# Performance work log

Hardware: AMD Instinct MI355X
Metric: run time of the kernel (lower is better)

Reference implementation:

```python
import jax, jax.numpy as jnp
import numpy as np

# Static multi-level feature-map geometry (h, w) per level.
SPATIAL_SHAPES = np.array([[92, 92], [46, 46], [23, 23], [12, 12]], dtype=np.int32)
_AREAS = SPATIAL_SHAPES[:, 0] * SPATIAL_SHAPES[:, 1]
LEVEL_START = np.concatenate([[0], np.cumsum(_AREAS)[:-1]]).astype(np.int32)
LEN_IN = int(_AREAS.sum())  # 11253
N_HEADS, N_LEVELS, N_POINTS = 8, 4, 4
D_MODEL, D_HEAD = 256, 64


def setup_inputs() -> dict:
    key = jax.random.key(0)
    ks = jax.random.split(key, 12)
    N, Lq = 4, 1000
    s = 0.02
    f32 = jnp.float32
    return {
        'query': jax.random.normal(ks[0], (N, Lq, D_MODEL), f32),
        'reference_points': jax.random.uniform(ks[1], (N, Lq, N_LEVELS, 2), f32),
        'input_flatten': jax.random.normal(ks[2], (N, LEN_IN, D_MODEL), f32),
        'input_spatial_shapes': jnp.asarray(SPATIAL_SHAPES),
        'input_level_start_index': jnp.asarray(LEVEL_START),
        'W_off': jax.random.normal(ks[3], (N_HEADS * N_LEVELS * N_POINTS * 2, D_MODEL), f32) * s,
        'b_off': jax.random.normal(ks[4], (N_HEADS * N_LEVELS * N_POINTS * 2,), f32) * 0.5,
        'W_attn': jax.random.normal(ks[5], (N_HEADS * N_LEVELS * N_POINTS, D_MODEL), f32) * s,
        'b_attn': jax.random.normal(ks[6], (N_HEADS * N_LEVELS * N_POINTS,), f32) * s,
        'W_val': jax.random.normal(ks[7], (N_HEADS * D_HEAD, D_MODEL), f32) * s,
        'b_val': jnp.zeros((N_HEADS * D_HEAD,), f32),
        'W_out': jax.random.normal(ks[8], (D_MODEL, N_HEADS * D_HEAD), f32) * s,
        'b_out': jnp.zeros((D_MODEL,), f32),
    }


def _ms_deform_attn(value, sampling_locations, attention_weights):
    # value: [N, Len_in, H, D]; locations: [N, Lq, H, L, P, 2] in [0,1];
    # weights: [N, Lq, H, L, P] -> out [N, Lq, H*D]
    N, _, H, D = value.shape
    Lq, L, P = sampling_locations.shape[1], sampling_locations.shape[3], sampling_locations.shape[4]
    out = jnp.zeros((N, H, Lq, D), value.dtype)
    for l in range(L):
        h, w = int(SPATIAL_SHAPES[l, 0]), int(SPATIAL_SHAPES[l, 1])
        st = int(LEVEL_START[l])
        # per-level value as [N*H, h*w, D]
        v = value[:, st:st + h * w].transpose(0, 2, 1, 3).reshape(N * H, h * w, D)
        loc = sampling_locations[:, :, :, l].transpose(0, 2, 1, 3, 4).reshape(N * H, Lq * P, 2)
        aw = attention_weights[:, :, :, l].transpose(0, 2, 1, 3).reshape(N * H, Lq * P)
        # grid_sample align_corners=False convention (matches CUDA kernel)
        x = loc[..., 0] * w - 0.5
        y = loc[..., 1] * h - 0.5
        x0 = jnp.floor(x)
        y0 = jnp.floor(y)
        lx, ly = x - x0, y - y0
        x0i = x0.astype(jnp.int32)
        y0i = y0.astype(jnp.int32)

        def gather(yi, xi):
            valid = ((xi >= 0) & (xi < w) & (yi >= 0) & (yi < h)).astype(v.dtype)
            idx = jnp.clip(yi, 0, h - 1) * w + jnp.clip(xi, 0, w - 1)
            g = jnp.take_along_axis(v, idx[..., None], axis=1)  # [N*H, Lq*P, D]
            return g * valid[..., None]

        sampled = (gather(y0i, x0i) * ((1 - lx) * (1 - ly))[..., None]
                   + gather(y0i, x0i + 1) * (lx * (1 - ly))[..., None]
                   + gather(y0i + 1, x0i) * ((1 - lx) * ly)[..., None]
                   + gather(y0i + 1, x0i + 1) * (lx * ly)[..., None])
        out = out + (sampled * aw[..., None]).reshape(N, H, Lq, P, D).sum(axis=3)
    return out.transpose(0, 2, 1, 3).reshape(N, Lq, H * D)


def reference(query, reference_points, input_flatten, input_spatial_shapes,
              input_level_start_index, W_off, b_off, W_attn, b_attn,
              W_val, b_val, W_out, b_out):
    N, Lq, _ = query.shape
    Lin = input_flatten.shape[1]
    H, L, P, D = N_HEADS, N_LEVELS, N_POINTS, D_HEAD
    value = (input_flatten @ W_val.T + b_val).reshape(N, Lin, H, D)
    off = (query @ W_off.T + b_off).reshape(N, Lq, H, L, P, 2)
    aw = jax.nn.softmax((query @ W_attn.T + b_attn).reshape(N, Lq, H, L * P), axis=-1)
    aw = aw.reshape(N, Lq, H, L, P)
    # offset normalizer is (w, h) per level
    norm = jnp.asarray(SPATIAL_SHAPES[:, ::-1].copy(), jnp.float32)  # [L, 2]
    loc = reference_points[:, :, None, :, None, :] + off / norm[None, None, None, :, None, :]
    out = _ms_deform_attn(value, loc, aw)
    return out @ W_out.T + b_out
```

## Files before the change

### kernel.cpp

```cpp
#include <hip/hip_runtime.h>


typedef __attribute__((ext_vector_type(4))) float f32x4;
typedef __attribute__((ext_vector_type(8))) short bf16x8;
typedef __attribute__((ext_vector_type(4))) short bf16x4;

static __device__ __forceinline__ unsigned short f2bf(float f) {
    unsigned u = __builtin_bit_cast(unsigned, f);
    u += 0x7FFFu + ((u >> 16) & 1u);
    return (unsigned short)(u >> 16);
}
static __device__ __forceinline__ float bflo(unsigned d) {
    return __builtin_bit_cast(float, d << 16);
}
static __device__ __forceinline__ float bfhi(unsigned d) {
    return __builtin_bit_cast(float, d & 0xffff0000u);
}
static __device__ __forceinline__ void gload_lds16(const void* g, void* l) {
    __builtin_amdgcn_global_load_lds(
        (const __attribute__((address_space(1))) void*)g,
        (__attribute__((address_space(3))) void*)l, 16, 0, 0);
}

__global__ __launch_bounds__(256)
void cvt_k(const float* __restrict__ s0, const float* __restrict__ s1,
           const float* __restrict__ s2, const float* __restrict__ s3,
           const float* __restrict__ s4, const float* __restrict__ s5,
           unsigned short* __restrict__ dst) {
    const size_t i8 = ((size_t)blockIdx.x * 256 + threadIdx.x) * 8;
    if (i8 >= 12907520u) return;
    const float* sp; size_t loc;
    if (i8 < 11523072u)      { sp = s0; loc = i8; }
    else if (i8 < 12547072u) { sp = s1; loc = i8 - 11523072u; }
    else if (i8 < 12612608u) { sp = s2; loc = i8 - 12547072u; }
    else if (i8 < 12645376u) { sp = s3; loc = i8 - 12612608u; }
    else if (i8 < 12776448u) { sp = s4; loc = i8 - 12645376u; }
    else                     { sp = s5; loc = i8 - 12776448u; }
    f32x4 a = *(const f32x4*)(sp + loc);
    f32x4 b = *(const f32x4*)(sp + loc + 4);
    bf16x8 r;
    r[0] = f2bf(a[0]); r[1] = f2bf(a[1]); r[2] = f2bf(a[2]); r[3] = f2bf(a[3]);
    r[4] = f2bf(b[0]); r[5] = f2bf(b[1]); r[6] = f2bf(b[2]); r[7] = f2bf(b[3]);
    *(bf16x8*)(dst + i8) = r;
}

template<int MODE>
__global__ __launch_bounds__(256)
void gemm_bf16_tn(const unsigned short* __restrict__ A,
                  const unsigned short* __restrict__ B,
                  const unsigned short* __restrict__ A2,
                  const unsigned short* __restrict__ B2,
                  const float* __restrict__ bias, const float* __restrict__ bias2,
                  const float* __restrict__ bias3,
                  void* __restrict__ Cv, void* __restrict__ Cv2,
                  int M, int N, int K) {
    __shared__ __align__(16) char smem[65536];

    const int tid = threadIdx.x, lane = tid & 63, w = tid >> 6;
    const int wm = w >> 1, wn = w & 1;

    const unsigned short* Ap = A;
    const unsigned short* Bp = B;
    bool vmode = false;
    int bm, bn;
    if (MODE == 3) {
        const int bid = blockIdx.x;
        if (bid < 1408) {
            vmode = true;
            const int xcd = bid & 7;
            const int j   = bid >> 3;
            bm = xcd * 44 + (j >> 2);
            bn = j & 3;
        } else {
            const int r = bid - 1408;
            bm = r & 31; bn = r >> 5;
            Ap = A2; Bp = B2;
            M = 4000; N = 384;
        }
    } else {
        bm = blockIdx.x; bn = blockIdx.y;
    }

    const int r8 = lane >> 3;
    const int colsrc = (((lane & 7) ^ r8) << 4);
    const char* pa[4]; const char* pb[4];
#pragma unroll
    for (int j = 0; j < 4; j++) {
        int ra = bm * 128 + j * 32 + w * 8 + r8; ra = ra < M ? ra : M - 1;
        int rb = bn * 128 + j * 32 + w * 8 + r8; rb = rb < N ? rb : N - 1;
        pa[j] = (const char*)Ap + (size_t)ra * ((size_t)K * 2) + colsrc;
        pb[j] = (const char*)Bp + (size_t)rb * ((size_t)K * 2) + colsrc;
    }
    const int ldso = w << 10;
    const int NT = K >> 6;

    f32x4 acc[4][4] = {};
    const int fr = lane & 15, fq = lane >> 4;
    const int k8b = fq << 4;
    const int swzR = (fr & 7) << 4;

#pragma unroll
    for (int j = 0; j < 4; j++) {
        gload_lds16(pa[j], smem + j * 4096 + ldso);
        gload_lds16(pb[j], smem + 16384 + j * 4096 + ldso);
    }
    __syncthreads();

    for (int t = 0; t < NT; ++t) {
        const int cur = (t & 1) << 15;
        if (t + 1 < NT) {
            const int nxt = ((t + 1) & 1) << 15;
            const int off = (t + 1) << 7;
#pragma unroll
            for (int j = 0; j < 4; j++) {
                gload_lds16(pa[j] + off, smem + nxt + j * 4096 + ldso);
                gload_lds16(pb[j] + off, smem + nxt + 16384 + j * 4096 + ldso);
            }
        }
#pragma unroll
        for (int kk = 0; kk < 2; ++kk) {
            const int ko = ((kk << 6) + k8b) ^ swzR;
            bf16x8 af[4], bv[4];
#pragma unroll
            for (int m = 0; m < 4; m++)
                af[m] = *(const bf16x8*)(smem + cur + ((wm * 64 + m * 16 + fr) << 7) + ko);
#pragma unroll
            for (int nn = 0; nn < 4; nn++)
                bv[nn] = *(const bf16x8*)(smem + cur + 16384 + ((wn * 64 + nn * 16 + fr) << 7) + ko);
#pragma unroll
            for (int m = 0; m < 4; m++)
#pragma unroll
                for (int nn = 0; nn < 4; nn++)
                    acc[m][nn] = __builtin_amdgcn_mfma_f32_16x16x32_bf16(
                        af[m], bv[nn], acc[m][nn], 0, 0, 0);
        }
        __syncthreads();
    }

    if (MODE == 0 || !vmode) {
        float* C = (MODE == 3) ? (float*)Cv2 : (float*)Cv;
        const float* b1 = (MODE == 3) ? bias2 : bias;
        const int crow0 = bm * 128 + wm * 64 + fq * 4;
        const int ccol0 = bn * 128 + wn * 64 + fr;
#pragma unroll
        for (int m = 0; m < 4; m++) {
#pragma unroll
            for (int nn = 0; nn < 4; nn++) {
                const int col = ccol0 + nn * 16;
                const float bv2 = (MODE == 3 && col >= 256) ? bias3[col - 256]
                                                            : b1[col];
#pragma unroll
                for (int j = 0; j < 4; j++) {
                    const int row = crow0 + m * 16 + j;
                    if (row < M) C[(size_t)row * N + col] = acc[m][nn][j] + bv2;
                }
            }
        }
    } else {
        unsigned short* tile = (unsigned short*)smem + (size_t)w * (64 * 68);
        const int hh = bn * 2 + wn;
        float bvs[4];
#pragma unroll
        for (int nn = 0; nn < 4; nn++) bvs[nn] = bias[hh * 64 + nn * 16 + fr];
#pragma unroll
        for (int m = 0; m < 4; m++)
#pragma unroll
            for (int nn = 0; nn < 4; nn++)
#pragma unroll
                for (int j = 0; j < 4; j++)
                    tile[(m * 16 + fq * 4 + j) * 68 + nn * 16 + fr] =
                        f2bf(acc[m][nn][j] + bvs[nn]);
        __syncthreads();
        unsigned short* VT = (unsigned short*)Cv;
        const int q4 = (lane & 15) * 4;
        const int prow = lane >> 4;
#pragma unroll
        for (int it = 0; it < 16; ++it) {
            const int pl = it * 4 + prow;
            const int pixg = bm * 128 + wm * 64 + pl;
            if (pixg < M) {
                const int n = pixg / 11253;
                const int pix = pixg - n * 11253;
                bf16x4 v = *(const bf16x4*)&tile[pl * 68 + q4];
                *(bf16x4*)(VT + ((size_t)(n * 8 + hh) * 11253 + pix) * 64 + q4) = v;
            }
        }
    }
}

__global__ __launch_bounds__(256)
void sample_k(const unsigned short* __restrict__ valueT,
              const float* __restrict__ refp,
              const float* __restrict__ fused,
              unsigned int* __restrict__ msout)
{
    const int bid = blockIdx.x;
    const int xcd = bid & 7;
    const int jj  = bid >> 3;
    const int sl  = jj / 250;
    const int qb  = jj - sl * 250;
    const int nh  = xcd * 4 + sl;
    const int q   = __builtin_amdgcn_readfirstlane(qb * 4 + (threadIdx.x >> 6));
    const int lane = threadIdx.x & 63;
    const int g    = lane >> 5;
    const int n = nh >> 3, h = nh & 7;
    const int nq = n * 1000 + q;

    const int p  = lane & 15;
    const int lv = p >> 2;
    const int W  = lv == 0 ? 92 : lv == 1 ? 46 : lv == 2 ? 23 : 12;
    const int st = lv == 0 ? 0 : lv == 1 ? 8464 : lv == 2 ? 10580 : 11109;

    const float lg = fused[(size_t)nq * 384 + 256 + h * 16 + p];
    float mx = lg;
#pragma unroll
    for (int sft = 1; sft < 16; sft <<= 1) mx = fmaxf(mx, __shfl_xor(mx, sft));
    const float e = __expf(lg - mx);
    float sum = e;
#pragma unroll
    for (int sft = 1; sft < 16; sft <<= 1) sum += __shfl_xor(sum, sft);
    const float a = e / sum;

    const float rx = refp[(size_t)nq * 8 + lv * 2 + 0];
    const float ry = refp[(size_t)nq * 8 + lv * 2 + 1];
    const float ox = fused[(size_t)nq * 384 + h * 32 + p * 2 + 0];
    const float oy = fused[(size_t)nq * 384 + h * 32 + p * 2 + 1];

    const float x = rx * (float)W + ox - 0.5f;
    const float y = ry * (float)W + oy - 0.5f;
    const float xf = floorf(x), yf = floorf(y);
    const int x0 = (int)xf, y0 = (int)yf;
    const float lx = x - xf, ly = y - yf;
    const int xb = min(max(x0, 0), W - 2);
    const int yb = min(max(y0, 0), W - 2);
    const float wx0 = (xb     == x0) ? (1.f - lx) : ((xb     == x0 + 1) ? lx : 0.f);
    const float wx1 = (xb + 1 == x0) ? (1.f - lx) : ((xb + 1 == x0 + 1) ? lx : 0.f);
    const float wy0 = (yb     == y0) ? (1.f - ly) : ((yb     == y0 + 1) ? ly : 0.f);
    const float wy1 = (yb + 1 == y0) ? (1.f - ly) : ((yb + 1 == y0 + 1) ? ly : 0.f);
    const int idx0v = st + yb * W + xb;
    const float wxs = (lane & 16) ? wx1 : wx0;
    const float wav = a * wxs * wy0;
    const float wbv = a * wxs * wy1;

    const unsigned int* vb =
        (const unsigned int*)valueT + (size_t)nh * 11253 * 32;

    float acc0 = 0.f, acc1 = 0.f;
    const int srcb = g << 4;
#pragma unroll
    for (int pp = 0; pp < 16; pp++) {
        const int Wc = pp < 4 ? 92 : pp < 8 ? 46 : pp < 12 ? 23 : 12;
        const int src = pp + srcb;
        const int   i0 = __shfl(idx0v, src);
        const float w0 = __shfl(wav,   src);
        const float w1 = __shfl(wbv,   src);
        const int   i1 = i0 + Wc;
        const unsigned d0 = vb[i0 * 32 + lane];
        const unsigned d1 = vb[i1 * 32 + lane];
        acc0 = fmaf(w0, bflo(d0), acc0);
        acc1 = fmaf(w0, bfhi(d0), acc1);
        acc0 = fmaf(w1, bflo(d1), acc0);
        acc1 = fmaf(w1, bfhi(d1), acc1);
    }

    acc0 += __shfl(acc0, lane ^ 32);
    acc1 += __shfl(acc1, lane ^ 32);
    if (lane < 32) {
        const unsigned u = (unsigned)f2bf(acc0) | ((unsigned)f2bf(acc1) << 16);
        msout[(size_t)nq * 256 + h * 32 + (lane & 31)] = u;
    }
}

extern "C" void kernel_launch(void* const* d_in, const int* in_sizes, int n_in,
                              void* d_out, int out_size, void* d_ws, size_t ws_size,
                              hipStream_t stream) {
    (void)in_sizes; (void)n_in; (void)out_size; (void)ws_size;

    const float* query  = (const float*)d_in[0];
    const float* refp   = (const float*)d_in[1];
    const float* inpf   = (const float*)d_in[2];
    const float* W_off  = (const float*)d_in[5];
    const float* b_off  = (const float*)d_in[6];
    const float* W_attn = (const float*)d_in[7];
    const float* b_attn = (const float*)d_in[8];
    const float* W_val  = (const float*)d_in[9];
    const float* b_val  = (const float*)d_in[10];
    const float* W_out  = (const float*)d_in[11];
    const float* b_out  = (const float*)d_in[12];
    float* out = (float*)d_out;

    char* ws = (char*)d_ws;
    unsigned short* bf = (unsigned short*)ws;
    unsigned short* inpfb   = bf;
    unsigned short* queryb  = bf + 11523072;
    unsigned short* W_offb  = bf + 12547072;
    unsigned short* W_valb  = bf + 12645376;
    unsigned short* W_outb  = bf + 12776448;
    unsigned short* valueT  = (unsigned short*)(ws + 25815040);
    float* fusedb = (float*)(ws + 71907328);
    unsigned int* msoutu = (unsigned int*)(ws + 78051328);
    unsigned short* msoutb = (unsigned short*)msoutu;

    cvt_k<<<6303, 256, 0, stream>>>(inpf, query, W_off, W_attn, W_val, W_out, bf);
    gemm_bf16_tn<3><<<1504, 256, 0, stream>>>(
        inpfb, W_valb, queryb, W_offb, b_val, b_off, b_attn,
        valueT, fusedb, 45012, 512, 256);
    sample_k<<<8000, 256, 0, stream>>>(valueT, refp, fusedb, msoutu);
    gemm_bf16_tn<0><<<dim3(32, 2), 256, 0, stream>>>(
        msoutb, W_outb, nullptr, nullptr, b_out, nullptr, nullptr,
        out, nullptr, 4000, 256, 512);
}
```

Baseline: 83.73 us.

## Fuse fp32-to-bf16 conversion into GEMM fragment loads, drop separate cvt kernel

Removes the standalone conversion kernel that turned all fp32 inputs and weights into bf16. The GEMMs now stream fp32 tiles directly into LDS with K-tiles of 32 and convert to bf16 with packed conversion instructions when building MFMA fragments. The B operand for the offset/attention projection is read straight from the two separate weight arrays instead of a concatenated bf16 copy. The sampling kernel writes its output in fp32 so the output GEMM can consume it the same way. This removes a kernel launch and an extra full read and write of the large input. In exchange the GEMM loads twice the bytes per K element, doubles its loop trip count, and does conversion work inside the inner loop.

```diff
diff --git a/kernel.cpp b/kernel.cpp
--- a/kernel.cpp
+++ b/kernel.cpp
@@ -2,6 +2,7 @@
 
 
 typedef __attribute__((ext_vector_type(4))) float f32x4;
+typedef __attribute__((ext_vector_type(4))) unsigned int u32x4;
 typedef __attribute__((ext_vector_type(8))) short bf16x8;
 typedef __attribute__((ext_vector_type(4))) short bf16x4;
 
@@ -16,51 +17,41 @@
 static __device__ __forceinline__ float bfhi(unsigned d) {
     return __builtin_bit_cast(float, d & 0xffff0000u);
 }
+static __device__ __forceinline__ unsigned cvtpk(float lo, float hi) {
+    unsigned r;
+    asm("v_cvt_pk_bf16_f32 %0, %1, %2" : "=v"(r) : "v"(lo), "v"(hi));
+    return r;
+}
 static __device__ __forceinline__ void gload_lds16(const void* g, void* l) {
     __builtin_amdgcn_global_load_lds(
         (const __attribute__((address_space(1))) void*)g,
         (__attribute__((address_space(3))) void*)l, 16, 0, 0);
 }
 
-__global__ __launch_bounds__(256)
-void cvt_k(const float* __restrict__ s0, const float* __restrict__ s1,
-           const float* __restrict__ s2, const float* __restrict__ s3,
-           const float* __restrict__ s4, const float* __restrict__ s5,
-           unsigned short* __restrict__ dst) {
-    const size_t i8 = ((size_t)blockIdx.x * 256 + threadIdx.x) * 8;
-    if (i8 >= 12907520u) return;
-    const float* sp; size_t loc;
-    if (i8 < 11523072u)      { sp = s0; loc = i8; }
-    else if (i8 < 12547072u) { sp = s1; loc = i8 - 11523072u; }
-    else if (i8 < 12612608u) { sp = s2; loc = i8 - 12547072u; }
-    else if (i8 < 12645376u) { sp = s3; loc = i8 - 12612608u; }
-    else if (i8 < 12776448u) { sp = s4; loc = i8 - 12645376u; }
-    else                     { sp = s5; loc = i8 - 12776448u; }
-    f32x4 a = *(const f32x4*)(sp + loc);
-    f32x4 b = *(const f32x4*)(sp + loc + 4);
-    bf16x8 r;
-    r[0] = f2bf(a[0]); r[1] = f2bf(a[1]); r[2] = f2bf(a[2]); r[3] = f2bf(a[3]);
-    r[4] = f2bf(b[0]); r[5] = f2bf(b[1]); r[6] = f2bf(b[2]); r[7] = f2bf(b[3]);
-    *(bf16x8*)(dst + i8) = r;
+static __device__ __forceinline__ bf16x8 frag_f32(const char* base, int R,
+                                                  int fq, int fr7) {
+    const f32x4 x0 = *(const f32x4*)(base + (R << 7) + ((((fq << 1) | 0) ^ fr7) << 4));
+    const f32x4 x1 = *(const f32x4*)(base + (R << 7) + ((((fq << 1) | 1) ^ fr7) << 4));
+    u32x4 u = { cvtpk(x0[0], x0[1]), cvtpk(x0[2], x0[3]),
+                cvtpk(x1[0], x1[1]), cvtpk(x1[2], x1[3]) };
+    return __builtin_bit_cast(bf16x8, u);
 }
 
 template<int MODE>
 __global__ __launch_bounds__(256)
-void gemm_bf16_tn(const unsigned short* __restrict__ A,
-                  const unsigned short* __restrict__ B,
-                  const unsigned short* __restrict__ A2,
-                  const unsigned short* __restrict__ B2,
-                  const float* __restrict__ bias, const float* __restrict__ bias2,
-                  const float* __restrict__ bias3,
-                  void* __restrict__ Cv, void* __restrict__ Cv2,
-                  int M, int N, int K) {
+void gemm_k(const float* __restrict__ A,   const float* __restrict__ B,
+            const float* __restrict__ A2,  const float* __restrict__ B2a,
+            const float* __restrict__ B2b,
+            const float* __restrict__ bias, const float* __restrict__ bias2,
+            const float* __restrict__ bias3,
+            void* __restrict__ Cv, void* __restrict__ Cv2,
+            int M, int N, int K) {
     __shared__ __align__(16) char smem[65536];
 
     const int tid = threadIdx.x, lane = tid & 63, w = tid >> 6;
     const int wm = w >> 1, wn = w & 1;
 
-    const unsigned short* Ap = A;
-    const unsigned short* Bp = B;
+    const float* Ap = A;
     bool vmode = false;
     int bm, bn;
     if (MODE == 3) {
@@ -74,7 +65,7 @@
         } else {
             const int r = bid - 1408;
             bm = r & 31; bn = r >> 5;
-            Ap = A2; Bp = B2;
+            Ap = A2;
             M = 4000; N = 384;
         }
     } else {
@@ -88,16 +79,17 @@
     for (int j = 0; j < 4; j++) {
         int ra = bm * 128 + j * 32 + w * 8 + r8; ra = ra < M ? ra : M - 1;
         int rb = bn * 128 + j * 32 + w * 8 + r8; rb = rb < N ? rb : N - 1;
-        pa[j] = (const char*)Ap + (size_t)ra * ((size_t)K * 2) + colsrc;
-        pb[j] = (const char*)Bp + (size_t)rb * ((size_t)K * 2) + colsrc;
+        const float* bs = (MODE == 3 && !vmode) ? B2a : B;
+        if (MODE == 3 && !vmode && rb >= 256) { bs = B2b; rb -= 256; }
+        pa[j] = (const char*)Ap + (size_t)ra * ((size_t)K * 4) + colsrc;
+        pb[j] = (const char*)bs + (size_t)rb * ((size_t)K * 4) + colsrc;
     }
     const int ldso = w << 10;
-    const int NT = K >> 6;
+    const int NT = K >> 5;
 
     f32x4 acc[4][4] = {};
     const int fr = lane & 15, fq = lane >> 4;
-    const int k8b = fq << 4;
-    const int swzR = (fr & 7) << 4;
+    const int fr7 = fr & 7;
 
 #pragma unroll
     for (int j = 0; j < 4; j++) {
@@ -117,23 +109,19 @@
                 gload_lds16(pb[j] + off, smem + nxt + 16384 + j * 4096 + ldso);
             }
         }
-#pragma unroll
-        for (int kk = 0; kk < 2; ++kk) {
-            const int ko = ((kk << 6) + k8b) ^ swzR;
-            bf16x8 af[4], bv[4];
-#pragma unroll
-            for (int m = 0; m < 4; m++)
-                af[m] = *(const bf16x8*)(smem + cur + ((wm * 64 + m * 16 + fr) << 7) + ko);
+        bf16x8 af[4], bv[4];
+#pragma unroll
+        for (int m = 0; m < 4; m++)
+            af[m] = frag_f32(smem + cur, wm * 64 + m * 16 + fr, fq, fr7);
+#pragma unroll
+        for (int nn = 0; nn < 4; nn++)
+            bv[nn] = frag_f32(smem + cur + 16384, wn * 64 + nn * 16 + fr, fq, fr7);
+#pragma unroll
+        for (int m = 0; m < 4; m++)
 #pragma unroll
             for (int nn = 0; nn < 4; nn++)
-                bv[nn] = *(const bf16x8*)(smem + cur + 16384 + ((wn * 64 + nn * 16 + fr) << 7) + ko);
-#pragma unroll
-            for (int m = 0; m < 4; m++)
-#pragma unroll
-                for (int nn = 0; nn < 4; nn++)
-                    acc[m][nn] = __builtin_amdgcn_mfma_f32_16x16x32_bf16(
-                        af[m], bv[nn], acc[m][nn], 0, 0, 0);
-        }
+                acc[m][nn] = __builtin_amdgcn_mfma_f32_16x16x32_bf16(
+                    af[m], bv[nn], acc[m][nn], 0, 0, 0);
         __syncthreads();
     }
 
@@ -192,7 +180,7 @@
 void sample_k(const unsigned short* __restrict__ valueT,
               const float* __restrict__ refp,
               const float* __restrict__ fused,
-              unsigned int* __restrict__ msout)
+              float* __restrict__ msout)
 {
     const int bid = blockIdx.x;
     const int xcd = bid & 7;
@@ -266,8 +254,8 @@
     acc0 += __shfl(acc0, lane ^ 32);
     acc1 += __shfl(acc1, lane ^ 32);
     if (lane < 32) {
-        const unsigned u = (unsigned)f2bf(acc0) | ((unsigned)f2bf(acc1) << 16);
-        msout[(size_t)nq * 256 + h * 32 + (lane & 31)] = u;
+        float2 v2 = make_float2(acc0, acc1);
+        *(float2*)&msout[(size_t)nq * 512 + h * 64 + (lane & 31) * 2] = v2;
     }
 }
 
@@ -290,23 +278,15 @@
     float* out = (float*)d_out;
 
     char* ws = (char*)d_ws;
-    unsigned short* bf = (unsigned short*)ws;
-    unsigned short* inpfb   = bf;
-    unsigned short* queryb  = bf + 11523072;
-    unsigned short* W_offb  = bf + 12547072;
-    unsigned short* W_valb  = bf + 12645376;
-    unsigned short* W_outb  = bf + 12776448;
-    unsigned short* valueT  = (unsigned short*)(ws + 25815040);
-    float* fusedb = (float*)(ws + 71907328);
-    unsigned int* msoutu = (unsigned int*)(ws + 78051328);
-    unsigned short* msoutb = (unsigned short*)msoutu;
-
-    cvt_k<<<6303, 256, 0, stream>>>(inpf, query, W_off, W_attn, W_val, W_out, bf);
-    gemm_bf16_tn<3><<<1504, 256, 0, stream>>>(
-        inpfb, W_valb, queryb, W_offb, b_val, b_off, b_attn,
+    unsigned short* valueT = (unsigned short*)ws;
+    float* fusedb = (float*)(ws + 46092288);
+    float* msoutf = (float*)(ws + 52236288);
+
+    gemm_k<3><<<1504, 256, 0, stream>>>(
+        inpf, W_val, query, W_off, W_attn, b_val, b_off, b_attn,
         valueT, fusedb, 45012, 512, 256);
-    sample_k<<<8000, 256, 0, stream>>>(valueT, refp, fusedb, msoutu);
-    gemm_bf16_tn<0><<<dim3(32, 2), 256, 0, stream>>>(
-        msoutb, W_outb, nullptr, nullptr, b_out, nullptr, nullptr,
+    sample_k<<<8000, 256, 0, stream>>>(valueT, refp, fusedb, msoutf);
+    gemm_k<0><<<dim3(32, 2), 256, 0, stream>>>(
+        msoutf, W_out, nullptr, nullptr, nullptr, b_out, nullptr, nullptr,
         out, nullptr, 4000, 256, 512);
 }
```

Measured after the change: 84.49 us. Within noise of the previous version (+0.9%).
